# Optimization experiments

Hardware: AMD Instinct MI355X
Metric: run time of the kernel (lower is better)

## Reference

```python
import jax, jax.numpy as jnp
import numpy as np

BLOCK = 32          # MX_BLOCK_SIZE
SCALE_EMAX = 127.0  # scale_bits=8 -> shared exponent clamped to [-127, 127]


def _quantize_elem(x, ebits, mfrac, max_norm):
    """Quantize each element to a tiny float format (ebits exponent bits,
    mfrac fractional mantissa bits), round-half-to-even, saturate to max_norm."""
    ax = jnp.abs(x)
    priv = jnp.floor(jnp.log2(jnp.where(ax == 0, 1.0, ax)))
    min_exp = float(-(2 ** (ebits - 1)) + 2)  # subnormal flush exponent
    priv = jnp.maximum(priv, min_exp)
    scale = jnp.exp2(priv - mfrac)
    q = jnp.round(x / scale) * scale  # jnp.round is round-half-to-even
    return jnp.clip(q, -max_norm, max_norm)


def _quantize_mx(x, ebits, mfrac, emax_elem, max_norm):
    """MX block-floating-point quantization along the last axis.
    shared_exp = floor(log2(blockmax)) - emax_elem (shared_exp_method='max')."""
    shp = x.shape
    xb = x.reshape(shp[:-1] + (shp[-1] // BLOCK, BLOCK))
    amax = jnp.max(jnp.abs(xb), axis=-1, keepdims=True)
    sexp = jnp.floor(jnp.log2(jnp.where(amax == 0, 1.0, amax))) - emax_elem
    sexp = jnp.clip(sexp, -SCALE_EMAX, SCALE_EMAX)
    scale = jnp.exp2(sexp)
    q = _quantize_elem(xb / scale, ebits, mfrac, max_norm) * scale
    return q.reshape(shp)


def _q_act(x):
    # fp6_e2m3: ebits=2, 3 fractional mantissa bits, emax=2, max_norm=7.5
    return _quantize_mx(x, 2, 3.0, 2.0, 7.5)


def _q_w(w):
    # fp4_e2m1: ebits=2, 1 fractional mantissa bit, emax=2, max_norm=6.0
    return _quantize_mx(w, 2, 1.0, 2.0, 6.0)


def _mx_linear(x, w):
    # quantize activation (fp6) and weight (fp4) along the shared in_features axis,
    # then do the matmul in high precision (dequant-fused GEMM semantics).
    return jnp.einsum('bsh,oh->bso', _q_act(x), _q_w(w))


def setup_inputs() -> dict:
    key = jax.random.key(0)
    k1, k2, k3, k4 = jax.random.split(key, 4)
    B, S, H, I = 1, 4096, 2048, 8192
    x = jax.random.normal(k1, (B, S, H), dtype=jnp.float32)
    w_gate = jax.random.normal(k2, (I, H), dtype=jnp.float32) * 0.02
    w_up = jax.random.normal(k3, (I, H), dtype=jnp.float32) * 0.02
    w_down = jax.random.normal(k4, (H, I), dtype=jnp.float32) * 0.02
    return {"x": x, "w_gate": w_gate, "w_up": w_up, "w_down": w_down}


def reference(x, w_gate, w_up, w_down):
    gate = _mx_linear(x, w_gate)            # [B, S, I]
    up = _mx_linear(x, w_up)                # [B, S, I]
    inter = jax.nn.silu(gate) * up          # SwiGLU
    return _mx_linear(inter, w_down)        # [B, S, H]
```

## Files before the change

### kernel.cpp

```cpp
#include <hip/hip_runtime.h>
#include <hip/hip_bf16.h>

typedef __attribute__((ext_vector_type(4))) int i32x4;
typedef __attribute__((ext_vector_type(8))) int i32x8;
typedef __attribute__((ext_vector_type(4))) float f32x4;

__device__ __forceinline__ int flog2(float x) {
  unsigned u = __float_as_uint(x);
  int e = (int)((u >> 23) & 255u);
  if (e) return e - 127;
  unsigned m = u & 0x7fffffu;
  return (31 - __clz(m)) - 149;
}

__device__ __forceinline__ float exp2i(int e) {
  int e1 = e >> 1, e2 = e - e1;
  return __uint_as_float((unsigned)(e1 + 127) << 23) *
         __uint_as_float((unsigned)(e2 + 127) << 23);
}

template <int MFRAC>
__device__ __forceinline__ float qelem(float y, float maxn) {
  float ay = fabsf(y);
  int e = (ay == 0.f) ? 0 : flog2(ay);
  if (e < 0) e = 0;
  float r = rintf(y * exp2i(MFRAC - e)) * exp2i(e - MFRAC);
  return fminf(fmaxf(r, -maxn), maxn);
}

__device__ __forceinline__ unsigned char enc_rne(float v) {
  unsigned u = __float_as_uint(v);
  unsigned s = u >> 31;
  float a = fabsf(v);
  if (a == 0.f) return (unsigned char)(s << 7);
  int e = flog2(a);
  if (e < -6) e = -6;
  int qi = (int)rintf(a * exp2i(3 - e));
  if (qi == 0) return (unsigned char)(s << 7);
  if (qi == 16) { qi = 8; e += 1; }
  unsigned exf, m;
  if (qi < 8) { exf = 0u; m = (unsigned)qi; }
  else { exf = (unsigned)(e + 7); m = (unsigned)(qi - 8); }
  return (unsigned char)((s << 7) | (exf << 3) | m);
}

__device__ __forceinline__ size_t swz(int row, int col, int pa) {
  return ((size_t)((row >> 4) * pa + (col >> 7))) * 2048
       + (size_t)((((row & 15) + (((col >> 5) & 3) << 4)) << 5) + (col & 31));
}

template <int MFRAC, int EMAX>
__global__ void quant_fold(const float* __restrict__ in, unsigned char* __restrict__ out,
                           long n4, float maxn, int se0, int kshift, int kmask, int pa) {
  long i = (long)blockIdx.x * blockDim.x + threadIdx.x;
  long stride = (long)gridDim.x * blockDim.x;
  for (; i < n4; i += stride) {
    float4 v = reinterpret_cast<const float4*>(in)[i];
    float am = fmaxf(fmaxf(fabsf(v.x), fabsf(v.y)), fmaxf(fabsf(v.z), fabsf(v.w)));
    am = fmaxf(am, __shfl_xor(am, 1));
    am = fmaxf(am, __shfl_xor(am, 2));
    am = fmaxf(am, __shfl_xor(am, 4));
    int se = ((am == 0.f) ? 0 : flog2(am)) - EMAX;
    se = se < -127 ? -127 : (se > 127 ? 127 : se);
    float inv = exp2i(-se), f = exp2i(se - se0);
    unsigned o = (unsigned)enc_rne(qelem<MFRAC>(v.x * inv, maxn) * f)
               | ((unsigned)enc_rne(qelem<MFRAC>(v.y * inv, maxn) * f) << 8)
               | ((unsigned)enc_rne(qelem<MFRAC>(v.z * inv, maxn) * f) << 16)
               | ((unsigned)enc_rne(qelem<MFRAC>(v.w * inv, maxn) * f) << 24);
    int row = (int)(i >> kshift);
    int kq = ((int)i & kmask) * 4;
    reinterpret_cast<unsigned*>(out)[swz(row, kq, pa) >> 2] = o;
  }
}

__device__ __forceinline__ i32x8 gfrag(const unsigned char* page, int l32) {
  return *reinterpret_cast<const i32x8*>(page + l32);
}

__global__ __launch_bounds__(256, 2) void mx_gateup(
    const unsigned char* __restrict__ A, int pa,
    const unsigned char* __restrict__ Bg, const unsigned char* __restrict__ Bu, int pb,
    unsigned char* __restrict__ C8, int ldC, float fac, int se0out, int nby) {
  const int t = threadIdx.x, l = t & 63, w = t >> 6;
  const int wr = w >> 1, wc = w & 1;
  const int lr16 = l & 15, lg16 = l >> 4;
  const int l32 = l * 32;
  const int n = (int)blockIdx.x;
  const int bx = n % 32, by = n / 32;
  const int rowA = bx * 128, rowB = by * 128;
  const int SCL = 0x7f7f7f7f;

  f32x4 accg[4][4], accu[4][4];
#pragma unroll
  for (int i = 0; i < 4; ++i)
#pragma unroll
    for (int j = 0; j < 4; ++j) { accg[i][j] = (f32x4)(0.f); accu[i][j] = (f32x4)(0.f); }

  const unsigned char* pApg[4];
  const unsigned char* pBg[4];
  const unsigned char* pBu[4];
#pragma unroll
  for (int m = 0; m < 4; ++m) {
    pApg[m] = A + (size_t)((rowA >> 4) + wr * 4 + m) * pa * 2048;
    pBg[m] = Bg + (size_t)((rowB >> 4) + wc * 4 + m) * pb * 2048;
    pBu[m] = Bu + (size_t)((rowB >> 4) + wc * 4 + m) * pb * 2048;
  }

  const int nt = pa;
#pragma unroll 2
  for (int kb = 0; kb < nt; ++kb) {
    i32x8 af[4], bg[4], bu[4];
#pragma unroll
    for (int m = 0; m < 4; ++m) { af[m] = gfrag(pApg[m], l32); pApg[m] += 2048; }
#pragma unroll
    for (int m = 0; m < 4; ++m) { bg[m] = gfrag(pBg[m], l32); pBg[m] += 2048; }
#pragma unroll
    for (int m = 0; m < 4; ++m) { bu[m] = gfrag(pBu[m], l32); pBu[m] += 2048; }
#pragma unroll
    for (int m = 0; m < 4; ++m)
#pragma unroll
      for (int nn = 0; nn < 4; ++nn) {
        accg[m][nn] = __builtin_amdgcn_mfma_scale_f32_16x16x128_f8f6f4(
            af[m], bg[nn], accg[m][nn], 0, 0, 0, SCL, 0, SCL);
        accu[m][nn] = __builtin_amdgcn_mfma_scale_f32_16x16x128_f8f6f4(
            af[m], bu[nn], accu[m][nn], 0, 0, 0, SCL, 0, SCL);
      }
  }

  const int pao = ldC >> 7;
#pragma unroll
  for (int m = 0; m < 4; ++m)
#pragma unroll
    for (int p = 0; p < 2; ++p)
#pragma unroll
      for (int r = 0; r < 4; ++r) {
        int row = rowA + wr * 64 + m * 16 + lg16 * 4 + r;
        int col = rowB + wc * 64 + p * 32 + lr16;
        float g0 = accg[m][2 * p][r] * fac;
        float g1 = accg[m][2 * p + 1][r] * fac;
        float u0 = accu[m][2 * p][r] * fac;
        float u1 = accu[m][2 * p + 1][r] * fac;
        float v0 = u0 * (g0 / (1.f + expf(-g0)));
        float v1 = u1 * (g1 / (1.f + expf(-g1)));
        float am = fmaxf(fabsf(v0), fabsf(v1));
        am = fmaxf(am, __shfl_xor(am, 1));
        am = fmaxf(am, __shfl_xor(am, 2));
        am = fmaxf(am, __shfl_xor(am, 4));
        am = fmaxf(am, __shfl_xor(am, 8));
        int se = ((am == 0.f) ? 0 : flog2(am)) - 2;
        se = se < -127 ? -127 : (se > 127 ? 127 : se);
        float f = exp2i(-se), fo = exp2i(se - se0out);
        C8[swz(row, col, pao)] = enc_rne(qelem<3>(v0 * f, 7.5f) * fo);
        C8[swz(row, col + 16, pao)] = enc_rne(qelem<3>(v1 * f, 7.5f) * fo);
      }
}

__global__ __launch_bounds__(256, 2) void mx_down(
    const unsigned char* __restrict__ A, int pa,
    const unsigned char* __restrict__ B, int pb,
    float* __restrict__ Cf, float* __restrict__ Cf2,
    int K, int ldC, float fac, int nby) {
  const int t = threadIdx.x, l = t & 63, w = t >> 6;
  const int wr = w >> 1, wc = w & 1;
  const int lr16 = l & 15, lg16 = l >> 4;
  const int l32 = l * 32;
  const int n = (int)blockIdx.x;
  const int bx = n & 31, byks = n >> 5;
  const int by = byks % nby, ks = byks / nby;
  const int rowA = bx * 128, rowB = by * 256;
  const int kbs = ks * (K >> 7);
  const int SCL = 0x7f7f7f7f;

  f32x4 acc[4][8];
#pragma unroll
  for (int i = 0; i < 4; ++i)
#pragma unroll
    for (int j = 0; j < 8; ++j) acc[i][j] = (f32x4)(0.f);

  const unsigned char* pApg[4];
  const unsigned char* pBpg[8];
#pragma unroll
  for (int m = 0; m < 4; ++m)
    pApg[m] = A + ((size_t)((rowA >> 4) + wr * 4 + m) * pa + kbs) * 2048;
#pragma unroll
  for (int nn = 0; nn < 8; ++nn)
    pBpg[nn] = B + ((size_t)((rowB >> 4) + wc * 8 + nn) * pb + kbs) * 2048;

  const int nt = K >> 7;
#pragma unroll 2
  for (int kb = 0; kb < nt; ++kb) {
    i32x8 af[4], bf[8];
#pragma unroll
    for (int m = 0; m < 4; ++m) { af[m] = gfrag(pApg[m], l32); pApg[m] += 2048; }
#pragma unroll
    for (int nn = 0; nn < 8; ++nn) { bf[nn] = gfrag(pBpg[nn], l32); pBpg[nn] += 2048; }
#pragma unroll
    for (int m = 0; m < 4; ++m)
#pragma unroll
      for (int nn = 0; nn < 8; ++nn)
        acc[m][nn] = __builtin_amdgcn_mfma_scale_f32_16x16x128_f8f6f4(
            af[m], bf[nn], acc[m][nn], 0, 0, 0, SCL, 0, SCL);
  }

  float* D = ks ? Cf2 : Cf;
#pragma unroll
  for (int m = 0; m < 4; ++m)
#pragma unroll
    for (int nn = 0; nn < 8; ++nn)
#pragma unroll
      for (int r = 0; r < 4; ++r) {
        int row = rowA + wr * 64 + m * 16 + lg16 * 4 + r;
        int col = rowB + wc * 128 + nn * 16 + lr16;
        D[(size_t)row * ldC + col] = acc[m][nn][r] * fac;
      }
}

__global__ void add_f32(float* __restrict__ out, const float* __restrict__ part, long n4) {
  long i = (long)blockIdx.x * blockDim.x + threadIdx.x;
  long stride = (long)gridDim.x * blockDim.x;
  for (; i < n4; i += stride) {
    float4 a = reinterpret_cast<float4*>(out)[i];
    float4 b = reinterpret_cast<const float4*>(part)[i];
    a.x += b.x; a.y += b.y; a.z += b.z; a.w += b.w;
    reinterpret_cast<float4*>(out)[i] = a;
  }
}

extern "C" void kernel_launch(void* const* d_in, const int* in_sizes, int n_in,
                              void* d_out, int out_size, void* d_ws, size_t ws_size,
                              hipStream_t stream) {
  const float* x = (const float*)d_in[0];
  const float* wg = (const float*)d_in[1];
  const float* wu = (const float*)d_in[2];
  const float* wd = (const float*)d_in[3];
  float* out = (float*)d_out;

  const int S = 4096, H = 2048, I = 8192;

  const int SE0X = -1, SE0W = -7, SE0I = -2;
  const float FAC_GU = 0.00390625f;
  const float FAC_DN = 0.001953125f;

  unsigned char* p = (unsigned char*)d_ws;
  unsigned char* xq8 = p;  p += (size_t)S * H;
  unsigned char* wgq8 = p; p += (size_t)I * H;
  unsigned char* wuq8 = p; p += (size_t)I * H;
  unsigned char* wdq8 = p; p += (size_t)H * I;
  unsigned char* iq8 = p;  p += (size_t)S * I;
  float* pf = (float*)p;

  quant_fold<3, 2><<<2048, 256, 0, stream>>>(x, xq8, (long)S * H / 4, 7.5f, SE0X,
                                             9, 511, H / 128);
  quant_fold<1, 2><<<2048, 256, 0, stream>>>(wg, wgq8, (long)I * H / 4, 6.0f, SE0W,
                                             9, 511, H / 128);
  quant_fold<1, 2><<<2048, 256, 0, stream>>>(wu, wuq8, (long)I * H / 4, 6.0f, SE0W,
                                             9, 511, H / 128);
  quant_fold<1, 2><<<2048, 256, 0, stream>>>(wd, wdq8, (long)H * I / 4, 6.0f, SE0W,
                                             11, 2047, I / 128);

  mx_gateup<<<32 * (I / 128), 256, 0, stream>>>(
      xq8, H / 128, wgq8, wuq8, H / 128, iq8, I, FAC_GU, SE0I, I / 128);

  mx_down<<<32 * (H / 256) * 2, 256, 0, stream>>>(
      iq8, I / 128, wdq8, I / 128, out, pf, I / 2, H, FAC_DN, H / 256);
  add_f32<<<2048, 256, 0, stream>>>(out, pf, (long)S * H / 4);
}
```

Measured before the change: 415.2 us.

## Remap GEMM block indices per XCD for L2 locality, add setprio and deeper unroll

Both GEMM kernels now decode blockIdx so that blocks landing on the same XCD (round-robin by n&7) share the same weight column tiles, improving L2 reuse of B fragments. The main loops are also unrolled 4 instead of 2, and the MFMA sections are wrapped in s_setprio raises so waves issuing matrix ops get scheduling priority. The mapping hardcodes the problem dimensions (64 by-tiles for gateup, 8x2 for down), trading generality for locality; the deeper unroll may increase register pressure.

```diff
diff --git a/kernel.cpp b/kernel.cpp
--- a/kernel.cpp
+++ b/kernel.cpp
@@ -80,21 +80,23 @@
 __global__ __launch_bounds__(256, 2) void mx_gateup(
     const unsigned char* __restrict__ A, int pa,
     const unsigned char* __restrict__ Bg, const unsigned char* __restrict__ Bu, int pb,
-    unsigned char* __restrict__ C8, int ldC, float fac, int se0out, int nby) {
+    unsigned char* __restrict__ C8, int ldC, float fac, int se0out) {
   const int t = threadIdx.x, l = t & 63, w = t >> 6;
   const int wr = w >> 1, wc = w & 1;
   const int lr16 = l & 15, lg16 = l >> 4;
   const int l32 = l * 32;
   const int n = (int)blockIdx.x;
-  const int bx = n % 32, by = n / 32;
+  const int xcd = n & 7, i = n >> 3;
+  const int bx = i & 31, byl = i >> 5;
+  const int by = xcd * 8 + byl;
   const int rowA = bx * 128, rowB = by * 128;
   const int SCL = 0x7f7f7f7f;
 
   f32x4 accg[4][4], accu[4][4];
 #pragma unroll
-  for (int i = 0; i < 4; ++i)
-#pragma unroll
-    for (int j = 0; j < 4; ++j) { accg[i][j] = (f32x4)(0.f); accu[i][j] = (f32x4)(0.f); }
+  for (int i2 = 0; i2 < 4; ++i2)
+#pragma unroll
+    for (int j = 0; j < 4; ++j) { accg[i2][j] = (f32x4)(0.f); accu[i2][j] = (f32x4)(0.f); }
 
   const unsigned char* pApg[4];
   const unsigned char* pBg[4];
@@ -107,7 +109,7 @@
   }
 
   const int nt = pa;
-#pragma unroll 2
+#pragma unroll 4
   for (int kb = 0; kb < nt; ++kb) {
     i32x8 af[4], bg[4], bu[4];
 #pragma unroll
@@ -116,6 +118,7 @@
     for (int m = 0; m < 4; ++m) { bg[m] = gfrag(pBg[m], l32); pBg[m] += 2048; }
 #pragma unroll
     for (int m = 0; m < 4; ++m) { bu[m] = gfrag(pBu[m], l32); pBu[m] += 2048; }
+    __builtin_amdgcn_s_setprio(1);
 #pragma unroll
     for (int m = 0; m < 4; ++m)
 #pragma unroll
@@ -125,6 +128,7 @@
         accu[m][nn] = __builtin_amdgcn_mfma_scale_f32_16x16x128_f8f6f4(
             af[m], bu[nn], accu[m][nn], 0, 0, 0, SCL, 0, SCL);
       }
+    __builtin_amdgcn_s_setprio(0);
   }
 
   const int pao = ldC >> 7;
@@ -159,23 +163,25 @@
     const unsigned char* __restrict__ A, int pa,
     const unsigned char* __restrict__ B, int pb,
     float* __restrict__ Cf, float* __restrict__ Cf2,
-    int K, int ldC, float fac, int nby) {
+    int K, int ldC, float fac) {
   const int t = threadIdx.x, l = t & 63, w = t >> 6;
   const int wr = w >> 1, wc = w & 1;
   const int lr16 = l & 15, lg16 = l >> 4;
   const int l32 = l * 32;
   const int n = (int)blockIdx.x;
-  const int bx = n & 31, byks = n >> 5;
-  const int by = byks % nby, ks = byks / nby;
+  const int xcd = n & 7, i = n >> 3;
+  const int bx = i & 31, slot = i >> 5;
+  const int byks = xcd * 2 + slot;
+  const int by = byks & 7, ks = byks >> 3;
   const int rowA = bx * 128, rowB = by * 256;
   const int kbs = ks * (K >> 7);
   const int SCL = 0x7f7f7f7f;
 
   f32x4 acc[4][8];
 #pragma unroll
-  for (int i = 0; i < 4; ++i)
-#pragma unroll
-    for (int j = 0; j < 8; ++j) acc[i][j] = (f32x4)(0.f);
+  for (int i2 = 0; i2 < 4; ++i2)
+#pragma unroll
+    for (int j = 0; j < 8; ++j) acc[i2][j] = (f32x4)(0.f);
 
   const unsigned char* pApg[4];
   const unsigned char* pBpg[8];
@@ -187,19 +193,21 @@
     pBpg[nn] = B + ((size_t)((rowB >> 4) + wc * 8 + nn) * pb + kbs) * 2048;
 
   const int nt = K >> 7;
-#pragma unroll 2
+#pragma unroll 4
   for (int kb = 0; kb < nt; ++kb) {
     i32x8 af[4], bf[8];
 #pragma unroll
     for (int m = 0; m < 4; ++m) { af[m] = gfrag(pApg[m], l32); pApg[m] += 2048; }
 #pragma unroll
     for (int nn = 0; nn < 8; ++nn) { bf[nn] = gfrag(pBpg[nn], l32); pBpg[nn] += 2048; }
+    __builtin_amdgcn_s_setprio(1);
 #pragma unroll
     for (int m = 0; m < 4; ++m)
 #pragma unroll
       for (int nn = 0; nn < 8; ++nn)
         acc[m][nn] = __builtin_amdgcn_mfma_scale_f32_16x16x128_f8f6f4(
             af[m], bf[nn], acc[m][nn], 0, 0, 0, SCL, 0, SCL);
+    __builtin_amdgcn_s_setprio(0);
   }
 
   float* D = ks ? Cf2 : Cf;
@@ -259,9 +267,9 @@
                                              11, 2047, I / 128);
 
   mx_gateup<<<32 * (I / 128), 256, 0, stream>>>(
-      xq8, H / 128, wgq8, wuq8, H / 128, iq8, I, FAC_GU, SE0I, I / 128);
-
-  mx_down<<<32 * (H / 256) * 2, 256, 0, stream>>>(
-      iq8, I / 128, wdq8, I / 128, out, pf, I / 2, H, FAC_DN, H / 256);
+      xq8, H / 128, wgq8, wuq8, H / 128, iq8, I, FAC_GU, SE0I);
+
+  mx_down<<<512, 256, 0, stream>>>(
+      iq8, I / 128, wdq8, I / 128, out, pf, I / 2, H, FAC_DN);
   add_f32<<<2048, 256, 0, stream>>>(out, pf, (long)S * H / 4);
 }
```

Result: no change. 415.0 us (-0.0%).

## Stage GEMM operand tiles in LDS with direct global-to-LDS loads and larger blocks

Applied to the files above, without the earlier changes.

Both MX GEMM kernels now use 512-thread blocks covering 256-row A tiles. Each k-step's A and B fragments are copied cooperatively into a 64KB shared buffer with global_load_lds, then each wave reads its fragments from LDS instead of from global memory. Sharing the staged tiles across waves is meant to cut redundant global and L2 traffic. In exchange it adds two block barriers per k-iteration with no double buffering, so load latency is no longer hidden. The 64KB of LDS per block may also limit occupancy.

```diff
diff --git a/kernel.cpp b/kernel.cpp
--- a/kernel.cpp
+++ b/kernel.cpp
@@ -73,21 +73,29 @@
   }
 }
 
-__device__ __forceinline__ i32x8 gfrag(const unsigned char* page, int l32) {
+__device__ __forceinline__ void gl_lds16(const unsigned char* g, unsigned char* l) {
+  __builtin_amdgcn_global_load_lds(
+      (const __attribute__((address_space(1))) void*)g,
+      (__attribute__((address_space(3))) void*)l, 16, 0, 0);
+}
+
+__device__ __forceinline__ i32x8 lfrag(const unsigned char* page, int l32) {
   return *reinterpret_cast<const i32x8*>(page + l32);
 }
 
-__global__ __launch_bounds__(256, 2) void mx_gateup(
+__global__ __launch_bounds__(512, 2) void mx_gateup(
     const unsigned char* __restrict__ A, int pa,
     const unsigned char* __restrict__ Bg, const unsigned char* __restrict__ Bu, int pb,
-    unsigned char* __restrict__ C8, int ldC, float fac, int se0out, int nby) {
+    unsigned char* __restrict__ C8, int ldC, float fac, int se0out) {
+  __shared__ __align__(16) unsigned char lds[32 * 2048];
   const int t = threadIdx.x, l = t & 63, w = t >> 6;
-  const int wr = w >> 1, wc = w & 1;
+  const int sr = w >> 1, sc = w & 1;
   const int lr16 = l & 15, lg16 = l >> 4;
   const int l32 = l * 32;
   const int n = (int)blockIdx.x;
-  const int bx = n % 32, by = n / 32;
-  const int rowA = bx * 128, rowB = by * 128;
+  const int bx = n & 15, by = n >> 4;
+  const int rowA = bx * 256 + sr * 64;
+  const int rowB = by * 128 + sc * 64;
   const int SCL = 0x7f7f7f7f;
 
   f32x4 accg[4][4], accu[4][4];
@@ -96,26 +104,35 @@
 #pragma unroll
     for (int j = 0; j < 4; ++j) { accg[i][j] = (f32x4)(0.f); accu[i][j] = (f32x4)(0.f); }
 
-  const unsigned char* pApg[4];
-  const unsigned char* pBg[4];
-  const unsigned char* pBu[4];
-#pragma unroll
-  for (int m = 0; m < 4; ++m) {
-    pApg[m] = A + (size_t)((rowA >> 4) + wr * 4 + m) * pa * 2048;
-    pBg[m] = Bg + (size_t)((rowB >> 4) + wc * 4 + m) * pb * 2048;
-    pBu[m] = Bu + (size_t)((rowB >> 4) + wc * 4 + m) * pb * 2048;
+  const unsigned char* gsrc[8];
+  int dstb[8];
+#pragma unroll
+  for (int i = 0; i < 8; ++i) {
+    int c = t + i * 512;
+    int p = c >> 7, off = (c & 127) * 16;
+    const unsigned char* base;
+    if (p < 16) base = A + (size_t)(bx * 16 + p) * pa * 2048;
+    else if (p < 24) base = Bg + (size_t)(by * 8 + (p - 16)) * pb * 2048;
+    else base = Bu + (size_t)(by * 8 + (p - 24)) * pb * 2048;
+    gsrc[i] = base + off;
+    dstb[i] = c * 16;
   }
 
   const int nt = pa;
-#pragma unroll 2
   for (int kb = 0; kb < nt; ++kb) {
+#pragma unroll
+    for (int i = 0; i < 8; ++i) {
+      gl_lds16(gsrc[i], &lds[dstb[i]]);
+      gsrc[i] += 2048;
+    }
+    __syncthreads();
     i32x8 af[4], bg[4], bu[4];
 #pragma unroll
-    for (int m = 0; m < 4; ++m) { af[m] = gfrag(pApg[m], l32); pApg[m] += 2048; }
-#pragma unroll
-    for (int m = 0; m < 4; ++m) { bg[m] = gfrag(pBg[m], l32); pBg[m] += 2048; }
-#pragma unroll
-    for (int m = 0; m < 4; ++m) { bu[m] = gfrag(pBu[m], l32); pBu[m] += 2048; }
+    for (int m = 0; m < 4; ++m) af[m] = lfrag(&lds[(sr * 4 + m) * 2048], l32);
+#pragma unroll
+    for (int m = 0; m < 4; ++m) bg[m] = lfrag(&lds[(16 + sc * 4 + m) * 2048], l32);
+#pragma unroll
+    for (int m = 0; m < 4; ++m) bu[m] = lfrag(&lds[(24 + sc * 4 + m) * 2048], l32);
 #pragma unroll
     for (int m = 0; m < 4; ++m)
 #pragma unroll
@@ -125,6 +142,7 @@
         accu[m][nn] = __builtin_amdgcn_mfma_scale_f32_16x16x128_f8f6f4(
             af[m], bu[nn], accu[m][nn], 0, 0, 0, SCL, 0, SCL);
       }
+    __syncthreads();
   }
 
   const int pao = ldC >> 7;
@@ -134,8 +152,8 @@
     for (int p = 0; p < 2; ++p)
 #pragma unroll
       for (int r = 0; r < 4; ++r) {
-        int row = rowA + wr * 64 + m * 16 + lg16 * 4 + r;
-        int col = rowB + wc * 64 + p * 32 + lr16;
+        int row = rowA + m * 16 + lg16 * 4 + r;
+        int col = rowB + p * 32 + lr16;
         float g0 = accg[m][2 * p][r] * fac;
         float g1 = accg[m][2 * p + 1][r] * fac;
         float u0 = accu[m][2 * p][r] * fac;
@@ -155,19 +173,21 @@
       }
 }
 
-__global__ __launch_bounds__(256, 2) void mx_down(
+__global__ __launch_bounds__(512, 2) void mx_down(
     const unsigned char* __restrict__ A, int pa,
     const unsigned char* __restrict__ B, int pb,
     float* __restrict__ Cf, float* __restrict__ Cf2,
-    int K, int ldC, float fac, int nby) {
+    int K, int ldC, float fac) {
+  __shared__ __align__(16) unsigned char lds[32 * 2048];
   const int t = threadIdx.x, l = t & 63, w = t >> 6;
-  const int wr = w >> 1, wc = w & 1;
+  const int sr = w >> 1, sc = w & 1;
   const int lr16 = l & 15, lg16 = l >> 4;
   const int l32 = l * 32;
   const int n = (int)blockIdx.x;
-  const int bx = n & 31, byks = n >> 5;
-  const int by = byks % nby, ks = byks / nby;
-  const int rowA = bx * 128, rowB = by * 256;
+  const int bx = n & 15, rest = n >> 4;
+  const int by = rest & 7, ks = rest >> 3;
+  const int rowA = bx * 256 + sr * 64;
+  const int rowB = by * 256 + sc * 128;
   const int kbs = ks * (K >> 7);
   const int SCL = 0x7f7f7f7f;
 
@@ -177,29 +197,39 @@
 #pragma unroll
     for (int j = 0; j < 8; ++j) acc[i][j] = (f32x4)(0.f);
 
-  const unsigned char* pApg[4];
-  const unsigned char* pBpg[8];
-#pragma unroll
-  for (int m = 0; m < 4; ++m)
-    pApg[m] = A + ((size_t)((rowA >> 4) + wr * 4 + m) * pa + kbs) * 2048;
-#pragma unroll
-  for (int nn = 0; nn < 8; ++nn)
-    pBpg[nn] = B + ((size_t)((rowB >> 4) + wc * 8 + nn) * pb + kbs) * 2048;
+  const unsigned char* gsrc[8];
+  int dstb[8];
+#pragma unroll
+  for (int i = 0; i < 8; ++i) {
+    int c = t + i * 512;
+    int p = c >> 7, off = (c & 127) * 16;
+    const unsigned char* base;
+    if (p < 16) base = A + ((size_t)(bx * 16 + p) * pa + kbs) * 2048;
+    else base = B + ((size_t)(by * 16 + (p - 16)) * pb + kbs) * 2048;
+    gsrc[i] = base + off;
+    dstb[i] = c * 16;
+  }
 
   const int nt = K >> 7;
-#pragma unroll 2
   for (int kb = 0; kb < nt; ++kb) {
+#pragma unroll
+    for (int i = 0; i < 8; ++i) {
+      gl_lds16(gsrc[i], &lds[dstb[i]]);
+      gsrc[i] += 2048;
+    }
+    __syncthreads();
     i32x8 af[4], bf[8];
 #pragma unroll
-    for (int m = 0; m < 4; ++m) { af[m] = gfrag(pApg[m], l32); pApg[m] += 2048; }
-#pragma unroll
-    for (int nn = 0; nn < 8; ++nn) { bf[nn] = gfrag(pBpg[nn], l32); pBpg[nn] += 2048; }
+    for (int m = 0; m < 4; ++m) af[m] = lfrag(&lds[(sr * 4 + m) * 2048], l32);
+#pragma unroll
+    for (int nn = 0; nn < 8; ++nn) bf[nn] = lfrag(&lds[(16 + sc * 8 + nn) * 2048], l32);
 #pragma unroll
     for (int m = 0; m < 4; ++m)
 #pragma unroll
       for (int nn = 0; nn < 8; ++nn)
         acc[m][nn] = __builtin_amdgcn_mfma_scale_f32_16x16x128_f8f6f4(
             af[m], bf[nn], acc[m][nn], 0, 0, 0, SCL, 0, SCL);
+    __syncthreads();
   }
 
   float* D = ks ? Cf2 : Cf;
@@ -209,8 +239,8 @@
     for (int nn = 0; nn < 8; ++nn)
 #pragma unroll
       for (int r = 0; r < 4; ++r) {
-        int row = rowA + wr * 64 + m * 16 + lg16 * 4 + r;
-        int col = rowB + wc * 128 + nn * 16 + lr16;
+        int row = rowA + m * 16 + lg16 * 4 + r;
+        int col = rowB + nn * 16 + lr16;
         D[(size_t)row * ldC + col] = acc[m][nn][r] * fac;
       }
 }
@@ -258,10 +288,10 @@
   quant_fold<1, 2><<<2048, 256, 0, stream>>>(wd, wdq8, (long)H * I / 4, 6.0f, SE0W,
                                              11, 2047, I / 128);
 
-  mx_gateup<<<32 * (I / 128), 256, 0, stream>>>(
-      xq8, H / 128, wgq8, wuq8, H / 128, iq8, I, FAC_GU, SE0I, I / 128);
-
-  mx_down<<<32 * (H / 256) * 2, 256, 0, stream>>>(
-      iq8, I / 128, wdq8, I / 128, out, pf, I / 2, H, FAC_DN, H / 256);
+  mx_gateup<<<16 * (I / 128), 512, 0, stream>>>(
+      xq8, H / 128, wgq8, wuq8, H / 128, iq8, I, FAC_GU, SE0I);
+
+  mx_down<<<256, 512, 0, stream>>>(
+      iq8, I / 128, wdq8, I / 128, out, pf, I / 2, H, FAC_DN);
   add_f32<<<2048, 256, 0, stream>>>(out, pf, (long)S * H / 4);
 }
```

After: 455.5 us. +9.7%, slower.
